# Kernel optimization log

Hardware: AMD Instinct MI355X
Metric: run time of the kernel (lower is better)

## Reference

```python
import jax, jax.numpy as jnp
import numpy as np

SIZE = 4096
N_ITER = 10
TEMP = 0.1


def setup_inputs() -> dict:
    key = jax.random.key(0)
    kx, kw = jax.random.split(key)
    x = jax.random.normal(kx, (4, 2048, SIZE), dtype=jnp.float32)
    weight = jax.random.normal(kw, (SIZE, SIZE), dtype=jnp.float32)
    r_prev = jnp.zeros((SIZE, 1), dtype=jnp.float32)
    c_prev = jnp.zeros((1, SIZE), dtype=jnp.float32)
    return {"x": x, "weight": weight, "r_prev": r_prev, "c_prev": c_prev}


def reference(x, weight, r_prev, c_prev):
    Q = weight / TEMP  # [S, S]

    def body(i, rc):
        r, c = rc
        r = -jax.nn.logsumexp(Q + c, axis=1, keepdims=True)  # [S, 1]
        c = -jax.nn.logsumexp(Q + r, axis=0, keepdims=True)  # [1, S]
        return (r, c)

    r, c = jax.lax.fori_loop(0, N_ITER, body, (r_prev, c_prev))
    P = jnp.exp(Q + r + c)  # doubly-stochastic-ish [S, S]
    # F.linear(x, P) == x @ P.T
    return jnp.einsum('btd,od->bto', x, P)
```

## Files before the change

kernel.cpp:

```cpp
#include <hip/hip_runtime.h>


#define L2E 1.44269504088896340736f

typedef __attribute__((ext_vector_type(8))) short bf16x8;
typedef __attribute__((ext_vector_type(4))) float f32x4;

__device__ __forceinline__ unsigned short f2bf(float x) {
  unsigned u = __float_as_uint(x);
  u += 0x7fffu + ((u >> 16) & 1u);
  return (unsigned short)(u >> 16);
}
__device__ __forceinline__ float bf2f(short x) {
  return __uint_as_float(((unsigned)(unsigned short)x) << 16);
}

__global__ void prep_e(const float* __restrict__ W, unsigned short* __restrict__ E) {
  const int row = blockIdx.x;
  const int t = threadIdx.x;
  const float* wp = W + ((size_t)row << 12);
  float v[16];
  float m = -3.4e38f;
#pragma unroll
  for (int ch = 0; ch < 4; ++ch) {
    float4 wv = *(const float4*)(wp + ch * 1024 + t * 4);
    float a0 = 10.f * wv.x, a1 = 10.f * wv.y, a2 = 10.f * wv.z, a3 = 10.f * wv.w;
    v[ch * 4 + 0] = a0; v[ch * 4 + 1] = a1; v[ch * 4 + 2] = a2; v[ch * 4 + 3] = a3;
    m = fmaxf(m, fmaxf(fmaxf(a0, a1), fmaxf(a2, a3)));
  }
#pragma unroll
  for (int off = 32; off > 0; off >>= 1) m = fmaxf(m, __shfl_xor(m, off));
  __shared__ float sm[4];
  if ((t & 63) == 0) sm[t >> 6] = m;
  __syncthreads();
  m = fmaxf(fmaxf(sm[0], sm[1]), fmaxf(sm[2], sm[3]));
  unsigned short* ep = E + ((size_t)row << 12);
#pragma unroll
  for (int ch = 0; ch < 4; ++ch) {
    ushort4 o;
    o.x = f2bf(exp2f((v[ch * 4 + 0] - m) * L2E));
    o.y = f2bf(exp2f((v[ch * 4 + 1] - m) * L2E));
    o.z = f2bf(exp2f((v[ch * 4 + 2] - m) * L2E));
    o.w = f2bf(exp2f((v[ch * 4 + 3] - m) * L2E));
    *(ushort4*)(ep + ch * 1024 + t * 4) = o;
  }
}

__global__ void transpose_bf(const unsigned short* __restrict__ E,
                             unsigned short* __restrict__ ET) {
  __shared__ unsigned short tile[64][66];
  const int t = threadIdx.x;
  const int r = t >> 3;
  const int c8 = (t & 7) << 3;
  const size_t i0 = (size_t)blockIdx.y << 6;
  const size_t j0 = (size_t)blockIdx.x << 6;
#pragma unroll
  for (int h = 0; h < 2; ++h) {
    bf16x8 vv = *(const bf16x8*)(E + (i0 + h * 32 + r) * 4096 + j0 + c8);
#pragma unroll
    for (int e = 0; e < 8; ++e) tile[h * 32 + r][c8 + e] = (unsigned short)vv[e];
  }
  __syncthreads();
#pragma unroll
  for (int h = 0; h < 2; ++h) {
    bf16x8 vv;
#pragma unroll
    for (int e = 0; e < 8; ++e) vv[e] = (short)tile[c8 + e][h * 32 + r];
    *(bf16x8*)(ET + (j0 + h * 32 + r) * 4096 + i0 + c8) = vv;
  }
}

__global__ void init_u(const float* __restrict__ c_prev, float* __restrict__ u) {
  const int i = blockIdx.x * 256 + threadIdx.x;
  u[i] = exp2f(c_prev[i] * L2E);
}

__global__ void recip_mv(const unsigned short* __restrict__ M,
                         const float* __restrict__ uin, float* __restrict__ vout) {
  const int t = threadIdx.x;
  const int l = t & 63, w = t >> 6;
  const int row = (blockIdx.x << 2) + w;
  const unsigned short* mp = M + ((size_t)row << 12);
  float s = 0.f;
#pragma unroll
  for (int ch = 0; ch < 8; ++ch) {
    const int j = (ch << 9) + (l << 3);
    bf16x8 e = *(const bf16x8*)(mp + j);
    const float4 u0 = *(const float4*)(uin + j);
    const float4 u1 = *(const float4*)(uin + j + 4);
    s = fmaf(bf2f(e[0]), u0.x, s);
    s = fmaf(bf2f(e[1]), u0.y, s);
    s = fmaf(bf2f(e[2]), u0.z, s);
    s = fmaf(bf2f(e[3]), u0.w, s);
    s = fmaf(bf2f(e[4]), u1.x, s);
    s = fmaf(bf2f(e[5]), u1.y, s);
    s = fmaf(bf2f(e[6]), u1.z, s);
    s = fmaf(bf2f(e[7]), u1.w, s);
  }
#pragma unroll
  for (int off = 32; off > 0; off >>= 1) s += __shfl_xor(s, off);
  if (l == 0) vout[row] = 1.f / s;
}

__global__ void scale_x(const float* __restrict__ X, const float* __restrict__ u,
                        unsigned short* __restrict__ Y) {
  const size_t idx = ((size_t)blockIdx.x * 256 + threadIdx.x) * 4;
  const int col = (int)(idx & 4095);
  float4 xv = *(const float4*)(X + idx);
  float4 uu = *(const float4*)(u + col);
  ushort4 o;
  o.x = f2bf(xv.x * uu.x);
  o.y = f2bf(xv.y * uu.y);
  o.z = f2bf(xv.z * uu.z);
  o.w = f2bf(xv.w * uu.w);
  *(ushort4*)(Y + idx) = o;
}

__global__ __launch_bounds__(512, 2) void gemm_bt(const unsigned short* __restrict__ A,
                                                  const unsigned short* __restrict__ B,
                                                  const float* __restrict__ vscale,
                                                  float* __restrict__ C) {
  __shared__ unsigned short lds[65536];
  const int t = threadIdx.x;
  const int l = t & 63;
  const int w = t >> 6;
  const int wm = w >> 2, wn = w & 3;

  int pid = blockIdx.x;
  pid = (pid & 7) * 64 + (pid >> 3);
  const int grp = pid >> 6;
  const int rem = pid & 63;
  const int bm = (grp << 2) + (rem & 3);
  const int bn = rem >> 2;
  const int m0 = bm << 8;
  const int n0 = bn << 8;

  const int ca = (((t & 3) ^ ((t >> 3) & 3)) << 3);
  const unsigned short* gA = A + (size_t)(m0 + (t >> 2)) * 4096 + ca;
  const unsigned short* gB = B + (size_t)(n0 + (t >> 2)) * 4096 + ca;

  const int xc = (((l >> 4) ^ ((l >> 1) & 3)) << 3);
  const int aOff = wm * 4096 + (l & 15) * 32 + xc;
  const int bOff = wn * 2048 + (l & 15) * 32 + xc;

  auto stage = [&](const unsigned short* gbase, int h, int isB) {
    const int slot = h & 3;
    const unsigned short* g = gbase + (size_t)h * 32;
#pragma unroll
    for (int ra = 0; ra < 2; ++ra)
      __builtin_amdgcn_global_load_lds(
          (const __attribute__((address_space(1))) void*)(g + (size_t)ra * 524288),
          (__attribute__((address_space(3))) void*)((char*)lds + isB * 65536 + slot * 16384 + ra * 8192 + w * 1024),
          16, 0, 0);
  };

  f32x4 acc[8][4] = {};
  bf16x8 afr[4], bfr[4];

  stage(gA, 0, 0); stage(gB, 0, 1);
  stage(gA, 1, 0); stage(gB, 1, 1);
  asm volatile("s_waitcnt vmcnt(4)" ::: "memory");
  __builtin_amdgcn_s_barrier();

#define PHASE(SLOT, MH, STAGE_STMT, WAIT_STMT)                                     \
  {                                                                                \
    const unsigned short* aL = lds + (SLOT) * 8192 + aOff + (MH) * 2048;           \
    _Pragma("unroll")                                                              \
    for (int i = 0; i < 4; ++i) afr[i] = *(const bf16x8*)(aL + i * 512);           \
    if ((MH) == 0) {                                                               \
      const unsigned short* bL = lds + 32768 + (SLOT) * 8192 + bOff;               \
      _Pragma("unroll")                                                            \
      for (int j = 0; j < 4; ++j) bfr[j] = *(const bf16x8*)(bL + j * 512);         \
    }                                                                              \
    STAGE_STMT;                                                                    \
    __builtin_amdgcn_s_barrier();                                                  \
    asm volatile("s_waitcnt lgkmcnt(0)" ::: "memory");                             \
    __builtin_amdgcn_sched_barrier(0);                                             \
    __builtin_amdgcn_s_setprio(1);                                                 \
    _Pragma("unroll")                                                              \
    for (int i = 0; i < 4; ++i)                                                    \
      _Pragma("unroll")                                                            \
      for (int j = 0; j < 4; ++j)                                                  \
        acc[(MH) * 4 + i][j] = __builtin_amdgcn_mfma_f32_16x16x32_bf16(            \
            afr[i], bfr[j], acc[(MH) * 4 + i][j], 0, 0, 0);                        \
    __builtin_amdgcn_s_setprio(0);                                                 \
    WAIT_STMT;                                                                     \
    __builtin_amdgcn_s_barrier();                                                  \
  }

  for (int kt = 0; kt < 64; kt += 2) {
    PHASE(0, 0, { if (kt <= 62) stage(gA, 2 * kt + 2, 0); }, {})
    PHASE(0, 1, { if (kt <= 62) stage(gB, 2 * kt + 2, 1); },
          { if (kt <= 62) asm volatile("s_waitcnt vmcnt(4)" ::: "memory");
            else          asm volatile("s_waitcnt vmcnt(0)" ::: "memory"); })
    PHASE(1, 0, { if (kt <= 62) stage(gA, 2 * kt + 3, 0); }, {})
    PHASE(1, 1, { if (kt <= 62) stage(gB, 2 * kt + 3, 1); },
          { if (kt <= 62) asm volatile("s_waitcnt vmcnt(4)" ::: "memory"); })
    PHASE(2, 0, { if (kt + 1 <= 62) stage(gA, 2 * kt + 4, 0); }, {})
    PHASE(2, 1, { if (kt + 1 <= 62) stage(gB, 2 * kt + 4, 1); },
          { if (kt + 1 <= 62) asm volatile("s_waitcnt vmcnt(4)" ::: "memory");
            else              asm volatile("s_waitcnt vmcnt(0)" ::: "memory"); })
    PHASE(3, 0, { if (kt + 1 <= 62) stage(gA, 2 * kt + 5, 0); }, {})
    PHASE(3, 1, { if (kt + 1 <= 62) stage(gB, 2 * kt + 5, 1); },
          { if (kt + 1 <= 62) asm volatile("s_waitcnt vmcnt(4)" ::: "memory"); })
  }
#undef PHASE

  const int crow = (l >> 4) << 2;
  const int ccol = l & 15;
#pragma unroll
  for (int j = 0; j < 4; ++j) {
    const int colj = n0 + (wn << 6) + (j << 4) + ccol;
    const float vs = vscale[colj];
#pragma unroll
    for (int i = 0; i < 8; ++i) {
      const int rowi = m0 + (wm << 7) + (i << 4) + crow;
#pragma unroll
      for (int q = 0; q < 4; ++q)
        C[((size_t)(rowi + q) << 12) + colj] = acc[i][j][q] * vs;
    }
  }
}

extern "C" void kernel_launch(void* const* d_in, const int* in_sizes, int n_in,
                              void* d_out, int out_size, void* d_ws, size_t ws_size,
                              hipStream_t stream) {
  const float* x      = (const float*)d_in[0];
  const float* weight = (const float*)d_in[1];
  const float* c_prev = (const float*)d_in[3];
  float* out = (float*)d_out;

  char* ws = (char*)d_ws;
  float* u = (float*)ws;
  float* v = (float*)(ws + (16 << 10));
  unsigned short* E  = (unsigned short*)(ws + (64 << 10));
  unsigned short* ET = E + (size_t)4096 * 4096;
  unsigned short* xb = ET;

  prep_e<<<4096, 256, 0, stream>>>(weight, E);
  transpose_bf<<<dim3(64, 64), 256, 0, stream>>>(E, ET);
  init_u<<<16, 256, 0, stream>>>(c_prev, u);

  for (int it = 0; it < 10; ++it) {
    recip_mv<<<1024, 256, 0, stream>>>(E, u, v);
    recip_mv<<<1024, 256, 0, stream>>>(ET, v, u);
  }

  scale_x<<<32768, 256, 0, stream>>>(x, u, xb);

  gemm_bt<<<512, 512, 0, stream>>>(xb, E, v, out);
}
```

Baseline: 436.4 us.

## Switch GEMM to 32x32x16 MFMA tiles and deepen LDS prefetch to three stages

Replaces the 16x16x32 bf16 MFMA with the 32x32x16 variant, so each wave computes 4x2 tiles of 32x32 with matching fragment offsets and a new epilogue index mapping. Fewer, larger MFMAs per k-step mean fewer LDS fragment reads per FLOP. The prefetch depth also grows from two to three stages in flight, with adjusted vmcnt waits, to hide more global-load latency. The change risks new LDS bank-conflict patterns from the altered swizzle reads and higher pressure on accumulator registers.

```diff
diff --git a/kernel.cpp b/kernel.cpp
--- a/kernel.cpp
+++ b/kernel.cpp
@@ -5,6 +5,7 @@
 
 typedef __attribute__((ext_vector_type(8))) short bf16x8;
 typedef __attribute__((ext_vector_type(4))) float f32x4;
+typedef __attribute__((ext_vector_type(16))) float f32x16;
 
 __device__ __forceinline__ unsigned short f2bf(float x) {
   unsigned u = __float_as_uint(x);
@@ -139,9 +140,11 @@
   const unsigned short* gA = A + (size_t)(m0 + (t >> 2)) * 4096 + ca;
   const unsigned short* gB = B + (size_t)(n0 + (t >> 2)) * 4096 + ca;
 
-  const int xc = (((l >> 4) ^ ((l >> 1) & 3)) << 3);
-  const int aOff = wm * 4096 + (l & 15) * 32 + xc;
-  const int bOff = wn * 2048 + (l & 15) * 32 + xc;
+  const int fl = (l >> 1) & 3;
+  const int ck0 = (((l >> 5) ^ fl) << 3);
+  const int ck1 = (((2 | (l >> 5)) ^ fl) << 3);
+  const int aBase = (wm * 128 + (l & 31)) * 32;
+  const int bBase = (wn * 64 + (l & 31)) * 32;
 
   auto stage = [&](const unsigned short* gbase, int h, int isB) {
     const int slot = h & 3;
@@ -154,70 +157,97 @@
           16, 0, 0);
   };
 
-  f32x4 acc[8][4] = {};
+  f32x16 acc[4][2] = {};
   bf16x8 afr[4], bfr[4];
 
   stage(gA, 0, 0); stage(gB, 0, 1);
   stage(gA, 1, 0); stage(gB, 1, 1);
-  asm volatile("s_waitcnt vmcnt(4)" ::: "memory");
+  stage(gA, 2, 0); stage(gB, 2, 1);
+  asm volatile("s_waitcnt vmcnt(8)" ::: "memory");
   __builtin_amdgcn_s_barrier();
 
-#define PHASE(SLOT, MH, STAGE_STMT, WAIT_STMT)                                     \
-  {                                                                                \
-    const unsigned short* aL = lds + (SLOT) * 8192 + aOff + (MH) * 2048;           \
-    _Pragma("unroll")                                                              \
-    for (int i = 0; i < 4; ++i) afr[i] = *(const bf16x8*)(aL + i * 512);           \
-    if ((MH) == 0) {                                                               \
-      const unsigned short* bL = lds + 32768 + (SLOT) * 8192 + bOff;               \
-      _Pragma("unroll")                                                            \
-      for (int j = 0; j < 4; ++j) bfr[j] = *(const bf16x8*)(bL + j * 512);         \
-    }                                                                              \
-    STAGE_STMT;                                                                    \
-    __builtin_amdgcn_s_barrier();                                                  \
-    asm volatile("s_waitcnt lgkmcnt(0)" ::: "memory");                             \
-    __builtin_amdgcn_sched_barrier(0);                                             \
-    __builtin_amdgcn_s_setprio(1);                                                 \
-    _Pragma("unroll")                                                              \
-    for (int i = 0; i < 4; ++i)                                                    \
-      _Pragma("unroll")                                                            \
-      for (int j = 0; j < 4; ++j)                                                  \
-        acc[(MH) * 4 + i][j] = __builtin_amdgcn_mfma_f32_16x16x32_bf16(            \
-            afr[i], bfr[j], acc[(MH) * 4 + i][j], 0, 0, 0);                        \
-    __builtin_amdgcn_s_setprio(0);                                                 \
-    WAIT_STMT;                                                                     \
-    __builtin_amdgcn_s_barrier();                                                  \
-  }
-
-  for (int kt = 0; kt < 64; kt += 2) {
-    PHASE(0, 0, { if (kt <= 62) stage(gA, 2 * kt + 2, 0); }, {})
-    PHASE(0, 1, { if (kt <= 62) stage(gB, 2 * kt + 2, 1); },
-          { if (kt <= 62) asm volatile("s_waitcnt vmcnt(4)" ::: "memory");
-            else          asm volatile("s_waitcnt vmcnt(0)" ::: "memory"); })
-    PHASE(1, 0, { if (kt <= 62) stage(gA, 2 * kt + 3, 0); }, {})
-    PHASE(1, 1, { if (kt <= 62) stage(gB, 2 * kt + 3, 1); },
-          { if (kt <= 62) asm volatile("s_waitcnt vmcnt(4)" ::: "memory"); })
-    PHASE(2, 0, { if (kt + 1 <= 62) stage(gA, 2 * kt + 4, 0); }, {})
-    PHASE(2, 1, { if (kt + 1 <= 62) stage(gB, 2 * kt + 4, 1); },
-          { if (kt + 1 <= 62) asm volatile("s_waitcnt vmcnt(4)" ::: "memory");
-            else              asm volatile("s_waitcnt vmcnt(0)" ::: "memory"); })
-    PHASE(3, 0, { if (kt + 1 <= 62) stage(gA, 2 * kt + 5, 0); }, {})
-    PHASE(3, 1, { if (kt + 1 <= 62) stage(gB, 2 * kt + 5, 1); },
-          { if (kt + 1 <= 62) asm volatile("s_waitcnt vmcnt(4)" ::: "memory"); })
-  }
-#undef PHASE
-
-  const int crow = (l >> 4) << 2;
-  const int ccol = l & 15;
-#pragma unroll
-  for (int j = 0; j < 4; ++j) {
-    const int colj = n0 + (wn << 6) + (j << 4) + ccol;
+#define MFMA32(a, b, c) __builtin_amdgcn_mfma_f32_32x32x16_bf16(a, b, c, 0, 0, 0)
+
+#define PH0(HV, SLOT)                                                          \
+  {                                                                            \
+    const unsigned short* aL = lds + (SLOT) * 8192 + aBase;                    \
+    const unsigned short* bL = lds + 32768 + (SLOT) * 8192 + bBase;            \
+    afr[0] = *(const bf16x8*)(aL + ck0);                                       \
+    afr[1] = *(const bf16x8*)(aL + ck1);                                       \
+    afr[2] = *(const bf16x8*)(aL + 1024 + ck0);                                \
+    afr[3] = *(const bf16x8*)(aL + 1024 + ck1);                                \
+    bfr[0] = *(const bf16x8*)(bL + ck0);                                       \
+    bfr[1] = *(const bf16x8*)(bL + ck1);                                       \
+    bfr[2] = *(const bf16x8*)(bL + 1024 + ck0);                                \
+    bfr[3] = *(const bf16x8*)(bL + 1024 + ck1);                                \
+    if ((HV) <= 124) stage(gA, (HV) + 3, 0);                                   \
+    __builtin_amdgcn_s_barrier();                                              \
+    asm volatile("s_waitcnt lgkmcnt(0)" ::: "memory");                         \
+    __builtin_amdgcn_sched_barrier(0);                                         \
+    __builtin_amdgcn_s_setprio(1);                                             \
+    acc[0][0] = MFMA32(afr[0], bfr[0], acc[0][0]);                             \
+    acc[0][1] = MFMA32(afr[0], bfr[2], acc[0][1]);                             \
+    acc[1][0] = MFMA32(afr[2], bfr[0], acc[1][0]);                             \
+    acc[1][1] = MFMA32(afr[2], bfr[2], acc[1][1]);                             \
+    acc[0][0] = MFMA32(afr[1], bfr[1], acc[0][0]);                             \
+    acc[0][1] = MFMA32(afr[1], bfr[3], acc[0][1]);                             \
+    acc[1][0] = MFMA32(afr[3], bfr[1], acc[1][0]);                             \
+    acc[1][1] = MFMA32(afr[3], bfr[3], acc[1][1]);                             \
+    __builtin_amdgcn_s_setprio(0);                                             \
+    __builtin_amdgcn_s_barrier();                                              \
+  }
+
+#define PH1(HV, SLOT)                                                          \
+  {                                                                            \
+    const unsigned short* aL = lds + (SLOT) * 8192 + aBase;                    \
+    afr[0] = *(const bf16x8*)(aL + 2048 + ck0);                                \
+    afr[1] = *(const bf16x8*)(aL + 2048 + ck1);                                \
+    afr[2] = *(const bf16x8*)(aL + 3072 + ck0);                                \
+    afr[3] = *(const bf16x8*)(aL + 3072 + ck1);                                \
+    if ((HV) <= 124) stage(gB, (HV) + 3, 1);                                   \
+    __builtin_amdgcn_s_barrier();                                              \
+    asm volatile("s_waitcnt lgkmcnt(0)" ::: "memory");                         \
+    __builtin_amdgcn_sched_barrier(0);                                         \
+    __builtin_amdgcn_s_setprio(1);                                             \
+    acc[2][0] = MFMA32(afr[0], bfr[0], acc[2][0]);                             \
+    acc[2][1] = MFMA32(afr[0], bfr[2], acc[2][1]);                             \
+    acc[3][0] = MFMA32(afr[2], bfr[0], acc[3][0]);                             \
+    acc[3][1] = MFMA32(afr[2], bfr[2], acc[3][1]);                             \
+    acc[2][0] = MFMA32(afr[1], bfr[1], acc[2][0]);                             \
+    acc[2][1] = MFMA32(afr[1], bfr[3], acc[2][1]);                             \
+    acc[3][0] = MFMA32(afr[3], bfr[1], acc[3][0]);                             \
+    acc[3][1] = MFMA32(afr[3], bfr[3], acc[3][1]);                             \
+    __builtin_amdgcn_s_setprio(0);                                             \
+    if ((HV) <= 124)      asm volatile("s_waitcnt vmcnt(8)" ::: "memory");     \
+    else if ((HV) == 125) asm volatile("s_waitcnt vmcnt(4)" ::: "memory");     \
+    else if ((HV) == 126) asm volatile("s_waitcnt vmcnt(0)" ::: "memory");     \
+    __builtin_amdgcn_s_barrier();                                              \
+  }
+
+  for (int h = 0; h < 128; h += 4) {
+    PH0(h + 0, 0) PH1(h + 0, 0)
+    PH0(h + 1, 1) PH1(h + 1, 1)
+    PH0(h + 2, 2) PH1(h + 2, 2)
+    PH0(h + 3, 3) PH1(h + 3, 3)
+  }
+#undef PH0
+#undef PH1
+#undef MFMA32
+
+  const int ccol = l & 31;
+  const int rbase = 4 * (l >> 5);
+#pragma unroll
+  for (int nj = 0; nj < 2; ++nj) {
+    const int colj = n0 + wn * 64 + nj * 32 + ccol;
     const float vs = vscale[colj];
 #pragma unroll
-    for (int i = 0; i < 8; ++i) {
-      const int rowi = m0 + (wm << 7) + (i << 4) + crow;
-#pragma unroll
-      for (int q = 0; q < 4; ++q)
-        C[((size_t)(rowi + q) << 12) + colj] = acc[i][j][q] * vs;
+    for (int mi = 0; mi < 4; ++mi) {
+      const int row0 = m0 + wm * 128 + mi * 32 + rbase;
+#pragma unroll
+      for (int r = 0; r < 16; ++r) {
+        const int rowi = row0 + (r & 3) + 8 * (r >> 2);
+        C[((size_t)rowi << 12) + colj] = acc[mi][nj][r] * vs;
+      }
     }
   }
 }
```

Measured after the change: 467.4 us. 1.07x slower.
